# Kernel tuning notes

Hardware: AMD Instinct MI355X
Metric: run time of the kernel (lower is better)

The kernel has to match this reference:

```python
import jax, jax.numpy as jnp
import numpy as np

N_RAYS, N_SAMPLES, N_VERTS = 2048, 32, 6890

def setup_inputs() -> dict:
    key = jax.random.key(0)
    k1, k2, k3, k4 = jax.random.split(key, 4)
    rays_points_world = jax.random.normal(k1, (1, N_RAYS, 1, N_SAMPLES, 3), jnp.float32)
    rays_directions_world = jax.random.normal(k2, (1, N_RAYS, 1, N_SAMPLES, 3), jnp.float32)
    vertices_posed = jax.random.normal(k3, (1, N_VERTS, 3), jnp.float32)
    # Ts must be invertible: small perturbation of identity (like rigid bone transforms)
    Ts = jax.random.normal(k4, (1, N_VERTS, 4, 4), jnp.float32) * 0.1 + jnp.eye(4, dtype=jnp.float32)
    return {
        'rays_points_world': rays_points_world,
        'rays_directions_world': rays_directions_world,
        'vertices_posed': vertices_posed,
        'Ts': Ts,
    }

def reference(rays_points_world, rays_directions_world, vertices_posed, Ts):
    orig_shape = rays_points_world.shape  # [1, R, 1, S, 3]
    pts = rays_points_world.reshape(-1, 3)          # (N, 3), N = R*S
    verts = vertices_posed[0]                       # (V, 3)
    # squared Euclidean distances via expansion (avoids N x V x 3 intermediate)
    d2 = ((pts * pts).sum(-1, keepdims=True)
          - 2.0 * (pts @ verts.T)
          + (verts * verts).sum(-1)[None, :])       # (N, V)
    idx = jnp.argmin(d2, axis=-1)                   # (N,) nearest vertex per point
    T_inv = jnp.linalg.inv(Ts)[0]                   # (V, 4, 4)
    T_sel = T_inv[idx]                              # (N, 4, 4) gather
    # flip x,y signs, build homogeneous coords
    xyz = jnp.stack([-pts[:, 0], -pts[:, 1], pts[:, 2]], axis=-1)      # (N, 3)
    homo = jnp.concatenate([xyz, jnp.ones_like(xyz[:, :1])], axis=-1)  # (N, 4)
    can = jnp.einsum('nij,nj->ni', T_sel, homo)[:, :3]                 # (N, 3)
    can = can.reshape(orig_shape)                                      # [1, R, 1, S, 3]
    # direction = finite diff along sample axis, last repeated
    dirs = can[..., 1:, :] - can[..., :-1, :]
    dirs = jnp.concatenate([dirs, dirs[..., -1:, :]], axis=-2)
    norm = jnp.linalg.norm(dirs, axis=-1, keepdims=True)
    dirs = dirs / jnp.maximum(norm, 1e-12)  # matches torch F.normalize eps
    flip = jnp.array([-1.0, -1.0, 1.0], dtype=can.dtype)
    return can * flip, dirs * flip
```

## Files before the change

kernel.cpp:

```cpp
#include <hip/hip_runtime.h>
#include <math.h>
#include <stdint.h>

#define N_RAYS    2048
#define N_SAMPLES 32
#define NPTS      (N_RAYS * N_SAMPLES)
#define NV        6890
#define G         32
#define NCELLS    (G * G * G)
#define SPLIT     8
#define RMAX      3
#define QMASK     0xFFFFE000u
#define IMASK     0x1FFFu
#define CMASK     0x1FFFu

#define TIE_REL   3e-3f
#define TIE_ABS   2e-5f

#define WS_COUNT     0
#define WS_FBC       4
#define WS_PARAMS    16
#define WS_HIST      128
#define WS_ROWMASK   (WS_HIST + 4 * NCELLS)
#define WS_CELLINFO  (WS_ROWMASK + 4 * G * G)
#define WS_SVERTS    (WS_CELLINFO + 4 * NCELLS)
#define WS_ORIGIDX   (WS_SVERTS + 16 * NV)
#define WS_LIST      (WS_ORIGIDX + 2 * NV + 12)
#define WS_NEEDED    (WS_LIST + 2 * NPTS)
#define WS_IDX       WS_HIST
#define WS_ZERO_W    ((WS_CELLINFO) / 4)

__device__ __forceinline__ uint64_t umin64(uint64_t a, uint64_t b) { return a < b ? a : b; }
__device__ __forceinline__ uint64_t umax64(uint64_t a, uint64_t b) { return a < b ? b : a; }

__global__ __launch_bounds__(256) void init_kernel(const float* __restrict__ verts,
                                                   float* __restrict__ params,
                                                   uint32_t* __restrict__ wzero) {
    const int t = threadIdx.x;
    if (blockIdx.x != 0) {
        for (int i = (blockIdx.x - 1) * 256 + t; i < WS_ZERO_W; i += (gridDim.x - 1) * 256) {
            if (i >= 4 && i < 32) continue;
            wzero[i] = 0u;
        }
        return;
    }
    __shared__ float mn[3][256], mx[3][256];
    float lmn[3] = {1e30f, 1e30f, 1e30f}, lmx[3] = {-1e30f, -1e30f, -1e30f};
    for (int v = t; v < NV; v += 256) {
        #pragma unroll
        for (int d = 0; d < 3; ++d) {
            float x = verts[v * 3 + d];
            lmn[d] = fminf(lmn[d], x); lmx[d] = fmaxf(lmx[d], x);
        }
    }
    #pragma unroll
    for (int d = 0; d < 3; ++d) { mn[d][t] = lmn[d]; mx[d][t] = lmx[d]; }
    __syncthreads();
    for (int s = 128; s > 0; s >>= 1) {
        if (t < s) {
            #pragma unroll
            for (int d = 0; d < 3; ++d) {
                mn[d][t] = fminf(mn[d][t], mn[d][t + s]);
                mx[d][t] = fmaxf(mx[d][t], mx[d][t + s]);
            }
        }
        __syncthreads();
    }
    if (t == 0) {
        #pragma unroll
        for (int d = 0; d < 3; ++d) {
            const float lo = mn[d][0] - 1e-3f, hi = mx[d][0] + 1e-3f;
            const float span = fmaxf(hi - lo, 1e-2f);
            params[d]     = lo;
            params[3 + d] = span / (float)G;
            params[6 + d] = (float)G / span;
        }
    }
}

__device__ __forceinline__ int cell_clamp(float x, float org, float ih) {
    int c = (int)floorf((x - org) * ih);
    return min(max(c, 0), G - 1);
}

__global__ void hist_kernel(const float* __restrict__ verts, const float* __restrict__ params,
                            uint32_t* __restrict__ hist) {
    const int v = blockIdx.x * blockDim.x + threadIdx.x;
    if (v >= NV) return;
    const int cx = cell_clamp(verts[v * 3 + 0], params[0], params[6]);
    const int cy = cell_clamp(verts[v * 3 + 1], params[1], params[7]);
    const int cz = cell_clamp(verts[v * 3 + 2], params[2], params[8]);
    atomicAdd(&hist[(cz * G + cy) * G + cx], 1u);
}

__global__ __launch_bounds__(1024) void scan_cells_kernel(const uint32_t* __restrict__ hist,
                                                          uint32_t* __restrict__ cellinfo,
                                                          uint32_t* __restrict__ rowmask) {
    __shared__ uint32_t part[1024];
    const int t = threadIdx.x;
    uint32_t loc[32];
    uint32_t sum = 0, rmask = 0;
    const int base = t * 32;
    #pragma unroll
    for (int i = 0; i < 32; ++i) {
        const uint32_t h = hist[base + i];
        loc[i] = sum; sum += h;
        if (h) rmask |= (1u << i);
    }
    part[t] = sum;
    rowmask[t] = rmask;
    __syncthreads();
    for (int off = 1; off < 1024; off <<= 1) {
        const uint32_t v = (t >= off) ? part[t - off] : 0u;
        __syncthreads();
        part[t] += v;
        __syncthreads();
    }
    const uint32_t pre = (t == 0) ? 0u : part[t - 1];
    #pragma unroll
    for (int i = 0; i < 32; ++i) {
        const uint32_t nxt = (i == 31) ? sum : loc[i + 1];
        const uint32_t cnt = nxt - loc[i];
        cellinfo[base + i] = ((pre + loc[i]) << 13) | cnt;
    }
}

__global__ void scatter_kernel(const float* __restrict__ verts, const float* __restrict__ params,
                               uint32_t* __restrict__ hist, const uint32_t* __restrict__ cellinfo,
                               float4* __restrict__ sverts, uint16_t* __restrict__ origidx) {
    const int v = blockIdx.x * blockDim.x + threadIdx.x;
    if (v >= NV) return;
    const float x = verts[v * 3 + 0], y = verts[v * 3 + 1], z = verts[v * 3 + 2];
    const int cx = cell_clamp(x, params[0], params[6]);
    const int cy = cell_clamp(y, params[1], params[7]);
    const int cz = cell_clamp(z, params[2], params[8]);
    const int c = (cz * G + cy) * G + cx;
    const uint32_t old = atomicSub(&hist[c], 1u);
    const uint32_t pos = (cellinfo[c] >> 13) + old - 1u;
    sverts[pos] = make_float4(x, y, z, fmaf(x, x, fmaf(y, y, z * z)));
    origidx[pos] = (uint16_t)v;
}

__global__ __launch_bounds__(256) void search_kernel(
    const float* __restrict__ pts, const float* __restrict__ params,
    const uint32_t* __restrict__ rowmask, const uint32_t* __restrict__ cellinfo,
    const float4* __restrict__ sverts, const uint16_t* __restrict__ origidx,
    uint16_t* __restrict__ idx16, uint16_t* __restrict__ list16,
    uint32_t* __restrict__ count, uint32_t* __restrict__ fbcount)
{
    __shared__ uint32_t srow[G * G];
    const int tid = threadIdx.x;
    for (int i = tid; i < G * G; i += 256) srow[i] = rowmask[i];
    __syncthreads();

    const int gtid = blockIdx.x * 256 + tid;
    const int sub  = gtid & (SPLIT - 1);
    const int n    = gtid / SPLIT;
    const float px = pts[n * 3 + 0], py = pts[n * 3 + 1], pz = pts[n * 3 + 2];
    const float acc = -0.5f * fmaf(px, px, fmaf(py, py, pz * pz));
    const float org0 = params[0], org1 = params[1], org2 = params[2];
    const float h0 = params[3], h1 = params[4], h2 = params[5];
    const int cx = cell_clamp(px, org0, params[6]);
    const int cy = cell_clamp(py, org1, params[7]);
    const int cz = cell_clamp(pz, org2, params[8]);

    uint32_t k1 = ~0u, k2 = ~0u;
    bool unproven = true;

    for (int r = 0; r <= RMAX; ++r) {
        const int xlo = max(cx - r, 0), xhi = min(cx + r, G - 1);
        const int ylo = max(cy - r, 0), yhi = min(cy + r, G - 1);
        const int zlo = max(cz - r, 0), zhi = min(cz + r, G - 1);
        const uint32_t wm = (uint32_t)((((uint64_t)1 << (xhi - xlo + 1)) - 1) << xlo);
        for (int z = zlo; z <= zhi; ++z) {
            const int az = abs(z - cz);
            for (int y = ylo; y <= yhi; ++y) {
                const int row = z * G + y;
                const int ayz = max(abs(y - cy), az);
                if (ayz == r) {
                    if (!(srow[row] & wm)) continue;
                    const uint32_t i0 = cellinfo[row * G + xlo];
                    const uint32_t i1 = cellinfo[row * G + xhi];
                    const uint32_t s = i0 >> 13;
                    const uint32_t e = (i1 >> 13) + (i1 & CMASK);
                    for (uint32_t j = s + sub; j < e; j += SPLIT) {
                        const float4 q = sverts[j];
                        const float dot = fmaf(px, q.x, fmaf(py, q.y, fmaf(pz, q.z, acc)));
                        const float d = fmaxf(fmaf(-2.f, dot, q.w), 0.f);
                        const uint32_t k = (__float_as_uint(d) & QMASK) | j;
                        k2 = min(k2, max(k1, k)); k1 = min(k1, k);
                    }
                } else {
                    #pragma unroll
                    for (int side = 0; side < 2; ++side) {
                        const int x = side ? cx + r : cx - r;
                        if (x < 0 || x > G - 1) continue;
                        if (!((srow[row] >> x) & 1u)) continue;
                        const uint32_t info = cellinfo[row * G + x];
                        const uint32_t s = info >> 13;
                        const uint32_t e = s + (info & CMASK);
                        for (uint32_t j = s + sub; j < e; j += SPLIT) {
                            const float4 q = sverts[j];
                            const float dot = fmaf(px, q.x, fmaf(py, q.y, fmaf(pz, q.z, acc)));
                            const float d = fmaxf(fmaf(-2.f, dot, q.w), 0.f);
                            const uint32_t k = (__float_as_uint(d) & QMASK) | j;
                            k2 = min(k2, max(k1, k)); k1 = min(k1, k);
                        }
                    }
                }
            }
        }
        uint32_t m1 = k1;
        #pragma unroll
        for (int off = 1; off < SPLIT; off <<= 1)
            m1 = min(m1, (uint32_t)__shfl_xor((int)m1, off));
        if (m1 != ~0u) {
            float dmin = 1e30f;
            bool any = false;
            if (xlo > 0)     { dmin = fminf(dmin, px - fmaf((float)xlo,     h0, org0)); any = true; }
            if (xhi < G - 1) { dmin = fminf(dmin, fmaf((float)(xhi + 1), h0, org0) - px); any = true; }
            if (ylo > 0)     { dmin = fminf(dmin, py - fmaf((float)ylo,     h1, org1)); any = true; }
            if (yhi < G - 1) { dmin = fminf(dmin, fmaf((float)(yhi + 1), h1, org1) - py); any = true; }
            if (zlo > 0)     { dmin = fminf(dmin, pz - fmaf((float)zlo,     h2, org2)); any = true; }
            if (zhi < G - 1) { dmin = fminf(dmin, fmaf((float)(zhi + 1), h2, org2) - pz); any = true; }
            if (!any) { unproven = false; break; }
            const float dout = fmaxf(dmin, 0.f);
            const float d1f = __uint_as_float(m1 & QMASK);
            if (dout * dout > fmaf(d1f, 1.05f, 1e-3f)) { unproven = false; break; }
        }
    }

    #pragma unroll
    for (int off = 1; off < SPLIT; off <<= 1) {
        const uint32_t o1 = (uint32_t)__shfl_xor((int)k1, off);
        const uint32_t o2 = (uint32_t)__shfl_xor((int)k2, off);
        k2 = min(min(k2, o2), max(k1, o1)); k1 = min(k1, o1);
    }

    if (sub == 0) {
        if (unproven) {
            const uint32_t p = atomicAdd(fbcount, 1u);
            list16[NPTS - 1 - p] = (uint16_t)n;
        } else {
            const float d1 = __uint_as_float(k1 & QMASK);
            const float d2 = __uint_as_float(k2 & QMASK);
            idx16[n] = origidx[k1 & IMASK];
            if (d2 - d1 < fmaf(TIE_REL, d1, TIE_ABS)) {
                const uint32_t p = atomicAdd(count, 1u);
                list16[p] = (uint16_t)n;
            }
        }
    }
}

__global__ __launch_bounds__(256) void fixup_kernel(
    const float* __restrict__ pts,
    const float4* __restrict__ sverts, const uint16_t* __restrict__ origidx,
    uint16_t* __restrict__ list16,
    const uint32_t* __restrict__ count, const uint32_t* __restrict__ fbcount,
    uint16_t* __restrict__ idx16)
{
    const uint32_t fcnt = *fbcount;
    const uint32_t tcnt = *count;
    const uint32_t total = fcnt + tcnt;
    const int wv = threadIdx.x >> 6, lane = threadIdx.x & 63;
    for (uint32_t jj = blockIdx.x * 4 + wv; jj < total; jj += gridDim.x * 4) {
        const bool isFb = jj < fcnt;
        const int n = isFb ? (int)list16[NPTS - 1 - jj] : (int)list16[jj - fcnt];
        const float px = pts[n * 3 + 0], py = pts[n * 3 + 1], pz = pts[n * 3 + 2];
        bool needF64 = true;
        if (isFb) {
            const float acc = -0.5f * fmaf(px, px, fmaf(py, py, pz * pz));
            uint32_t k1 = ~0u, k2 = ~0u;
            int v = lane;
            for (; v + 192 < NV; v += 256) {
                const float4 q0 = sverts[v];
                const float4 q1 = sverts[v + 64];
                const float4 q2 = sverts[v + 128];
                const float4 q3 = sverts[v + 192];
                float dot, d; uint32_t k;
                dot = fmaf(px, q0.x, fmaf(py, q0.y, fmaf(pz, q0.z, acc)));
                d = fmaxf(fmaf(-2.f, dot, q0.w), 0.f);
                k = (__float_as_uint(d) & QMASK) | (uint32_t)v;
                k2 = min(k2, max(k1, k)); k1 = min(k1, k);
                dot = fmaf(px, q1.x, fmaf(py, q1.y, fmaf(pz, q1.z, acc)));
                d = fmaxf(fmaf(-2.f, dot, q1.w), 0.f);
                k = (__float_as_uint(d) & QMASK) | (uint32_t)(v + 64);
                k2 = min(k2, max(k1, k)); k1 = min(k1, k);
                dot = fmaf(px, q2.x, fmaf(py, q2.y, fmaf(pz, q2.z, acc)));
                d = fmaxf(fmaf(-2.f, dot, q2.w), 0.f);
                k = (__float_as_uint(d) & QMASK) | (uint32_t)(v + 128);
                k2 = min(k2, max(k1, k)); k1 = min(k1, k);
                dot = fmaf(px, q3.x, fmaf(py, q3.y, fmaf(pz, q3.z, acc)));
                d = fmaxf(fmaf(-2.f, dot, q3.w), 0.f);
                k = (__float_as_uint(d) & QMASK) | (uint32_t)(v + 192);
                k2 = min(k2, max(k1, k)); k1 = min(k1, k);
            }
            for (; v < NV; v += 64) {
                const float4 q = sverts[v];
                const float dot = fmaf(px, q.x, fmaf(py, q.y, fmaf(pz, q.z, acc)));
                const float d = fmaxf(fmaf(-2.f, dot, q.w), 0.f);
                const uint32_t k = (__float_as_uint(d) & QMASK) | (uint32_t)v;
                k2 = min(k2, max(k1, k)); k1 = min(k1, k);
            }
            #pragma unroll
            for (int off = 1; off < 64; off <<= 1) {
                const uint32_t o1 = (uint32_t)__shfl_xor((int)k1, off);
                const uint32_t o2 = (uint32_t)__shfl_xor((int)k2, off);
                k2 = min(min(k2, o2), max(k1, o1)); k1 = min(k1, o1);
            }
            const float d1 = __uint_as_float(k1 & QMASK);
            const float d2 = __uint_as_float(k2 & QMASK);
            needF64 = (d2 - d1 < fmaf(TIE_REL, d1, TIE_ABS));
            if (!needF64 && lane == 0) idx16[n] = origidx[k1 & IMASK];
        }
        if (needF64) {
            const double pxd = (double)px, pyd = (double)py, pzd = (double)pz;
            double best = 1e300; uint32_t bi = 0xFFFFFFFFu;
            int v = lane;
            for (; v + 192 < NV; v += 256) {
                const float4 q0 = sverts[v];
                const float4 q1 = sverts[v + 64];
                const float4 q2 = sverts[v + 128];
                const float4 q3 = sverts[v + 192];
                const uint32_t o0 = origidx[v];
                const uint32_t o1 = origidx[v + 64];
                const uint32_t o2 = origidx[v + 128];
                const uint32_t o3 = origidx[v + 192];
                double dx, dy, dz, d;
                dx = pxd - (double)q0.x; dy = pyd - (double)q0.y; dz = pzd - (double)q0.z;
                d = dx*dx + dy*dy + dz*dz;
                if (d < best || (d == best && o0 < bi)) { best = d; bi = o0; }
                dx = pxd - (double)q1.x; dy = pyd - (double)q1.y; dz = pzd - (double)q1.z;
                d = dx*dx + dy*dy + dz*dz;
                if (d < best || (d == best && o1 < bi)) { best = d; bi = o1; }
                dx = pxd - (double)q2.x; dy = pyd - (double)q2.y; dz = pzd - (double)q2.z;
                d = dx*dx + dy*dy + dz*dz;
                if (d < best || (d == best && o2 < bi)) { best = d; bi = o2; }
                dx = pxd - (double)q3.x; dy = pyd - (double)q3.y; dz = pzd - (double)q3.z;
                d = dx*dx + dy*dy + dz*dz;
                if (d < best || (d == best && o3 < bi)) { best = d; bi = o3; }
            }
            for (; v < NV; v += 64) {
                const float4 q = sverts[v];
                const uint32_t oi = origidx[v];
                const double dx = pxd - (double)q.x;
                const double dy = pyd - (double)q.y;
                const double dz = pzd - (double)q.z;
                const double d = dx*dx + dy*dy + dz*dz;
                if (d < best || (d == best && oi < bi)) { best = d; bi = oi; }
            }
            #pragma unroll
            for (int off = 1; off < 64; off <<= 1) {
                const double od = __shfl_xor(best, off);
                const uint32_t oi = (uint32_t)__shfl_xor((int)bi, off);
                if (od < best || (od == best && oi < bi)) { best = od; bi = oi; }
            }
            if (lane == 0) idx16[n] = (uint16_t)bi;
        }
    }
}

__global__ __launch_bounds__(256) void output_kernel(
    const float* __restrict__ pts, const float* __restrict__ Ts,
    const uint16_t* __restrict__ idx16, float* __restrict__ out)
{
    __shared__ double sc[256][3];
    const int tid = threadIdx.x;
    const int n = blockIdx.x * 256 + tid;
    const float px = pts[n*3+0], py = pts[n*3+1], pz = pts[n*3+2];
    const int v = (int)idx16[n];

    const float4* T4 = reinterpret_cast<const float4*>(Ts + (size_t)v * 16);
    const float4 r0 = T4[0], r1 = T4[1], r2 = T4[2], r3 = T4[3];
    const double m[16] = { r0.x, r0.y, r0.z, r0.w,  r1.x, r1.y, r1.z, r1.w,
                           r2.x, r2.y, r2.z, r2.w,  r3.x, r3.y, r3.z, r3.w };
    double inv[16];
    inv[0]  =  m[5]*m[10]*m[15] - m[5]*m[11]*m[14] - m[9]*m[6]*m[15] + m[9]*m[7]*m[14] + m[13]*m[6]*m[11] - m[13]*m[7]*m[10];
    inv[4]  = -m[4]*m[10]*m[15] + m[4]*m[11]*m[14] + m[8]*m[6]*m[15] - m[8]*m[7]*m[14] - m[12]*m[6]*m[11] + m[12]*m[7]*m[10];
    inv[8]  =  m[4]*m[9]*m[15] - m[4]*m[11]*m[13] - m[8]*m[5]*m[15] + m[8]*m[7]*m[13] + m[12]*m[5]*m[11] - m[12]*m[7]*m[9];
    inv[12] = -m[4]*m[9]*m[14] + m[4]*m[10]*m[13] + m[8]*m[5]*m[14] - m[8]*m[6]*m[13] - m[12]*m[5]*m[10] + m[12]*m[6]*m[9];
    inv[1]  = -m[1]*m[10]*m[15] + m[1]*m[11]*m[14] + m[9]*m[2]*m[15] - m[9]*m[3]*m[14] - m[13]*m[2]*m[11] + m[13]*m[3]*m[10];
    inv[5]  =  m[0]*m[10]*m[15] - m[0]*m[11]*m[14] - m[8]*m[2]*m[15] + m[8]*m[3]*m[14] + m[12]*m[2]*m[11] - m[12]*m[3]*m[10];
    inv[9]  = -m[0]*m[9]*m[15] + m[0]*m[11]*m[13] + m[8]*m[1]*m[15] - m[8]*m[3]*m[13] - m[12]*m[1]*m[11] + m[12]*m[3]*m[9];
    inv[13] =  m[0]*m[9]*m[14] - m[0]*m[10]*m[13] - m[8]*m[1]*m[14] + m[8]*m[2]*m[13] + m[12]*m[1]*m[10] - m[12]*m[2]*m[9];
    inv[2]  =  m[1]*m[6]*m[15] - m[1]*m[7]*m[14] - m[5]*m[2]*m[15] + m[5]*m[3]*m[14] + m[13]*m[2]*m[7] - m[13]*m[3]*m[6];
    inv[6]  = -m[0]*m[6]*m[15] + m[0]*m[7]*m[14] + m[4]*m[2]*m[15] - m[4]*m[3]*m[14] - m[12]*m[2]*m[7] + m[12]*m[3]*m[6];
    inv[10] =  m[0]*m[5]*m[15] - m[0]*m[7]*m[13] - m[4]*m[1]*m[15] + m[4]*m[3]*m[13] + m[12]*m[1]*m[7] - m[12]*m[3]*m[5];
    inv[14] = -m[0]*m[5]*m[14] + m[0]*m[6]*m[13] + m[4]*m[1]*m[14] - m[4]*m[2]*m[13] - m[12]*m[1]*m[6] + m[12]*m[2]*m[5];
    inv[3]  = -m[1]*m[6]*m[11] + m[1]*m[7]*m[10] + m[5]*m[2]*m[11] - m[5]*m[3]*m[10] - m[9]*m[2]*m[7] + m[9]*m[3]*m[6];
    inv[7]  =  m[0]*m[6]*m[11] - m[0]*m[7]*m[10] - m[4]*m[2]*m[11] + m[4]*m[3]*m[10] + m[8]*m[2]*m[7] - m[8]*m[3]*m[6];
    inv[11] = -m[0]*m[5]*m[11] + m[0]*m[7]*m[9] + m[4]*m[1]*m[11] - m[4]*m[3]*m[9] - m[8]*m[1]*m[7] + m[8]*m[3]*m[5];
    inv[15] =  m[0]*m[5]*m[10] - m[0]*m[6]*m[9] - m[4]*m[1]*m[10] + m[4]*m[2]*m[9] + m[8]*m[1]*m[6] - m[8]*m[2]*m[5];
    const double det = m[0]*inv[0] + m[1]*inv[4] + m[2]*inv[8] + m[3]*inv[12];
    const double rd = 1.0 / det;

    const double hx = -(double)px, hy = -(double)py, hz = (double)pz;
    const double c0 = (inv[0]*hx + inv[1]*hy + inv[2]*hz  + inv[3])  * rd;
    const double c1 = (inv[4]*hx + inv[5]*hy + inv[6]*hz  + inv[7])  * rd;
    const double c2 = (inv[8]*hx + inv[9]*hy + inv[10]*hz + inv[11]) * rd;
    const double f0 = -c0, f1 = -c1, f2 = c2;

    out[n*3+0] = (float)f0; out[n*3+1] = (float)f1; out[n*3+2] = (float)f2;
    sc[tid][0] = f0; sc[tid][1] = f1; sc[tid][2] = f2;
    __syncthreads();

    int l0 = tid, l1 = tid + 1;
    if ((tid & (N_SAMPLES - 1)) == N_SAMPLES - 1) { l0 = tid - 1; l1 = tid; }
    const double dx = sc[l1][0] - sc[l0][0];
    const double dy = sc[l1][1] - sc[l0][1];
    const double dz = sc[l1][2] - sc[l0][2];
    const double nr = fmax(sqrt(dx*dx + dy*dy + dz*dz), 1e-12);
    float* o = out + (size_t)NPTS * 3 + (size_t)n * 3;
    o[0] = (float)(dx / nr); o[1] = (float)(dy / nr); o[2] = (float)(dz / nr);
}

__global__ void zero_kernel(uint32_t* __restrict__ w, int nwords) {
    for (int i = blockIdx.x * blockDim.x + threadIdx.x; i < nwords; i += gridDim.x * blockDim.x)
        w[i] = 0u;
}

__global__ __launch_bounds__(256) void scan_kernel(
    const float* __restrict__ pts, const float* __restrict__ verts,
    uint16_t* __restrict__ idx16, uint16_t* __restrict__ list16,
    uint32_t* __restrict__ count)
{
    __shared__ float4 sv[2048];
    const int tid  = threadIdx.x;
    const int part = tid & 7;
    const int grp  = tid >> 3;
    const int n0   = blockIdx.x * 64 + grp * 2;
    const float ax = pts[n0*3+0], ay = pts[n0*3+1], az = pts[n0*3+2];
    const float bx = pts[n0*3+3], by = pts[n0*3+4], bz = pts[n0*3+5];
    const float acc = -0.5f * fmaf(ax, ax, fmaf(ay, ay, az*az));
    const float bcc = -0.5f * fmaf(bx, bx, fmaf(by, by, bz*bz));
    uint64_t ak1 = ~0ull, ak2 = ~0ull, bk1 = ~0ull, bk2 = ~0ull;
    for (int base = 0; base < NV; base += 2048) {
        const int cnt = min(NV - base, 2048);
        __syncthreads();
        for (int v = tid; v < cnt; v += 256) {
            const float x = verts[(base+v)*3+0], y = verts[(base+v)*3+1], z = verts[(base+v)*3+2];
            sv[v] = make_float4(x, y, z, fmaf(x, x, fmaf(y, y, z*z)));
        }
        __syncthreads();
        #pragma unroll 4
        for (int v = part; v < cnt; v += 8) {
            const float4 q = sv[v];
            const uint64_t vi = (uint64_t)(base + v);
            float s, d; uint64_t k;
            s = fmaf(ax, q.x, fmaf(ay, q.y, fmaf(az, q.z, acc)));
            d = fmaxf(fmaf(-2.f, s, q.w), 0.f);
            k = ((uint64_t)__float_as_uint(d) << 32) | vi;
            ak2 = umin64(ak2, umax64(ak1, k)); ak1 = umin64(ak1, k);
            s = fmaf(bx, q.x, fmaf(by, q.y, fmaf(bz, q.z, bcc)));
            d = fmaxf(fmaf(-2.f, s, q.w), 0.f);
            k = ((uint64_t)__float_as_uint(d) << 32) | vi;
            bk2 = umin64(bk2, umax64(bk1, k)); bk1 = umin64(bk1, k);
        }
    }
    #pragma unroll
    for (int off = 1; off < 8; off <<= 1) {
        uint64_t o1, o2;
        o1 = __shfl_xor((unsigned long long)ak1, off); o2 = __shfl_xor((unsigned long long)ak2, off);
        ak2 = umin64(umin64(ak2, o2), umax64(ak1, o1)); ak1 = umin64(ak1, o1);
        o1 = __shfl_xor((unsigned long long)bk1, off); o2 = __shfl_xor((unsigned long long)bk2, off);
        bk2 = umin64(umin64(bk2, o2), umax64(bk1, o1)); bk1 = umin64(bk1, o1);
    }
    if (part == 0) {
        const float ad1 = __uint_as_float((uint32_t)(ak1 >> 32));
        const float ad2 = __uint_as_float((uint32_t)(ak2 >> 32));
        idx16[n0] = (uint16_t)(ak1 & 0xFFFFu);
        if (ad2 - ad1 < fmaf(1e-4f, ad1, TIE_ABS)) { uint32_t p = atomicAdd(count, 1u); list16[p] = (uint16_t)n0; }
        const float bd1 = __uint_as_float((uint32_t)(bk1 >> 32));
        const float bd2 = __uint_as_float((uint32_t)(bk2 >> 32));
        idx16[n0+1] = (uint16_t)(bk1 & 0xFFFFu);
        if (bd2 - bd1 < fmaf(1e-4f, bd1, TIE_ABS)) { uint32_t p = atomicAdd(count, 1u); list16[p] = (uint16_t)(n0+1); }
    }
}

__global__ __launch_bounds__(256) void refine_kernel(
    const float* __restrict__ pts, const float* __restrict__ verts,
    const uint16_t* __restrict__ list16, const uint32_t* __restrict__ count,
    uint16_t* __restrict__ idx16)
{
    const uint32_t cnt = *count;
    const int wv = threadIdx.x >> 6, lane = threadIdx.x & 63;
    for (uint32_t j = blockIdx.x * 4 + wv; j < cnt; j += gridDim.x * 4) {
        const int n = (int)list16[j];
        const double px = (double)pts[n*3+0];
        const double py = (double)pts[n*3+1];
        const double pz = (double)pts[n*3+2];
        double best = 1e300; uint32_t bi = 0xFFFFFFFFu;
        for (int v = lane; v < NV; v += 64) {
            const double dx = px - (double)verts[v*3+0];
            const double dy = py - (double)verts[v*3+1];
            const double dz = pz - (double)verts[v*3+2];
            const double d = dx*dx + dy*dy + dz*dz;
            if (d < best || (d == best && (uint32_t)v < bi)) { best = d; bi = (uint32_t)v; }
        }
        #pragma unroll
        for (int off = 1; off < 64; off <<= 1) {
            const double od = __shfl_xor(best, off);
            const uint32_t oi = (uint32_t)__shfl_xor((int)bi, off);
            if (od < best || (od == best && oi < bi)) { best = od; bi = oi; }
        }
        if (lane == 0) idx16[n] = (uint16_t)bi;
    }
}

extern "C" void kernel_launch(void* const* d_in, const int* in_sizes, int n_in,
                              void* d_out, int out_size, void* d_ws, size_t ws_size,
                              hipStream_t stream) {
    const float* pts   = (const float*)d_in[0];
    const float* verts = (const float*)d_in[2];
    const float* Ts    = (const float*)d_in[3];
    float* out = (float*)d_out;

    uint8_t* ws = (uint8_t*)d_ws;
    uint32_t* count   = (uint32_t*)(ws + WS_COUNT);
    uint32_t* fbcount = (uint32_t*)(ws + WS_FBC);

    if (ws_size >= (size_t)WS_NEEDED) {
        float*    params   = (float*)(ws + WS_PARAMS);
        uint32_t* hist     = (uint32_t*)(ws + WS_HIST);
        uint32_t* rowmask  = (uint32_t*)(ws + WS_ROWMASK);
        uint32_t* cellinfo = (uint32_t*)(ws + WS_CELLINFO);
        float4*   sverts   = (float4*)(ws + WS_SVERTS);
        uint16_t* origidx  = (uint16_t*)(ws + WS_ORIGIDX);
        uint16_t* idx16    = (uint16_t*)(ws + WS_IDX);
        uint16_t* list16   = (uint16_t*)(ws + WS_LIST);
        const int vblocks = (NV + 255) / 256;

        hipLaunchKernelGGL(init_kernel, dim3(65), dim3(256), 0, stream,
                           verts, params, (uint32_t*)ws);
        hipLaunchKernelGGL(hist_kernel, dim3(vblocks), dim3(256), 0, stream,
                           verts, params, hist);
        hipLaunchKernelGGL(scan_cells_kernel, dim3(1), dim3(1024), 0, stream,
                           hist, cellinfo, rowmask);
        hipLaunchKernelGGL(scatter_kernel, dim3(vblocks), dim3(256), 0, stream,
                           verts, params, hist, cellinfo, sverts, origidx);
        hipLaunchKernelGGL(search_kernel, dim3(NPTS * SPLIT / 256), dim3(256), 0, stream,
                           pts, params, rowmask, cellinfo, sverts, origidx,
                           idx16, list16, count, fbcount);
        hipLaunchKernelGGL(fixup_kernel, dim3(1024), dim3(256), 0, stream,
                           pts, sverts, origidx, list16, count, fbcount, idx16);
        hipLaunchKernelGGL(output_kernel, dim3(NPTS / 256), dim3(256), 0, stream,
                           pts, Ts, idx16, out);
    } else {
        uint16_t* idx16  = (uint16_t*)(ws + 64);
        uint16_t* list16 = (uint16_t*)(ws + 64 + 2 * NPTS);
        hipLaunchKernelGGL(zero_kernel, dim3(1), dim3(64), 0, stream, (uint32_t*)ws, 1);
        hipLaunchKernelGGL(scan_kernel, dim3(NPTS / 64), dim3(256), 0, stream,
                           pts, verts, idx16, list16, count);
        hipLaunchKernelGGL(refine_kernel, dim3(512), dim3(256), 0, stream,
                           pts, verts, list16, count, idx16);
        hipLaunchKernelGGL(output_kernel, dim3(NPTS / 256), dim3(256), 0, stream,
                           pts, Ts, idx16, out);
    }
}
```

Before: 85.74 us.

## Widen per-point split to 16 lanes and search grid in two shell stages

Each query point is now scanned by 16 lanes instead of 8, and the radius-by-radius shell search (r=0..3) becomes two stages. The first stage scans the 3x3x3 neighbourhood and checks whether the nearest vertex is proven. Only if not does a second stage scan the 7x7x7 box, skipping the already-scanned core. This cuts per-radius shuffle reductions and the loop overhead from the finer shells, and gives each lane fewer candidates. In exchange, unproven points scan the whole r=3 box at once, and the wider split doubles the thread count and adds a shuffle step to each reduction.

New measurement: 95.18 us. +11.0%, slower.

```diff
diff --git a/kernel.cpp b/kernel.cpp
--- a/kernel.cpp
+++ b/kernel.cpp
@@ -8,8 +8,7 @@
 #define NV        6890
 #define G         32
 #define NCELLS    (G * G * G)
-#define SPLIT     8
-#define RMAX      3
+#define SPLIT     16
 #define QMASK     0xFFFFE000u
 #define IMASK     0x1FFFu
 #define CMASK     0x1FFFu
@@ -32,6 +31,9 @@
 
 __device__ __forceinline__ uint64_t umin64(uint64_t a, uint64_t b) { return a < b ? a : b; }
 __device__ __forceinline__ uint64_t umax64(uint64_t a, uint64_t b) { return a < b ? b : a; }
+__device__ __forceinline__ uint32_t wmask(int a, int b) {
+    return (uint32_t)((((uint64_t)1 << (b - a + 1)) - 1) << a);
+}
 
 __global__ __launch_bounds__(256) void init_kernel(const float* __restrict__ verts,
                                                    float* __restrict__ params,
@@ -167,67 +169,72 @@
     uint32_t k1 = ~0u, k2 = ~0u;
     bool unproven = true;
 
-    for (int r = 0; r <= RMAX; ++r) {
-        const int xlo = max(cx - r, 0), xhi = min(cx + r, G - 1);
-        const int ylo = max(cy - r, 0), yhi = min(cy + r, G - 1);
-        const int zlo = max(cz - r, 0), zhi = min(cz + r, G - 1);
-        const uint32_t wm = (uint32_t)((((uint64_t)1 << (xhi - xlo + 1)) - 1) << xlo);
-        for (int z = zlo; z <= zhi; ++z) {
-            const int az = abs(z - cz);
-            for (int y = ylo; y <= yhi; ++y) {
-                const int row = z * G + y;
-                const int ayz = max(abs(y - cy), az);
-                if (ayz == r) {
-                    if (!(srow[row] & wm)) continue;
-                    const uint32_t i0 = cellinfo[row * G + xlo];
-                    const uint32_t i1 = cellinfo[row * G + xhi];
-                    const uint32_t s = i0 >> 13;
-                    const uint32_t e = (i1 >> 13) + (i1 & CMASK);
-                    for (uint32_t j = s + sub; j < e; j += SPLIT) {
-                        const float4 q = sverts[j];
-                        const float dot = fmaf(px, q.x, fmaf(py, q.y, fmaf(pz, q.z, acc)));
-                        const float d = fmaxf(fmaf(-2.f, dot, q.w), 0.f);
-                        const uint32_t k = (__float_as_uint(d) & QMASK) | j;
-                        k2 = min(k2, max(k1, k)); k1 = min(k1, k);
-                    }
-                } else {
-                    #pragma unroll
-                    for (int side = 0; side < 2; ++side) {
-                        const int x = side ? cx + r : cx - r;
-                        if (x < 0 || x > G - 1) continue;
-                        if (!((srow[row] >> x) & 1u)) continue;
-                        const uint32_t info = cellinfo[row * G + x];
-                        const uint32_t s = info >> 13;
-                        const uint32_t e = s + (info & CMASK);
-                        for (uint32_t j = s + sub; j < e; j += SPLIT) {
-                            const float4 q = sverts[j];
-                            const float dot = fmaf(px, q.x, fmaf(py, q.y, fmaf(pz, q.z, acc)));
-                            const float d = fmaxf(fmaf(-2.f, dot, q.w), 0.f);
-                            const uint32_t k = (__float_as_uint(d) & QMASK) | j;
-                            k2 = min(k2, max(k1, k)); k1 = min(k1, k);
-                        }
-                    }
-                }
-            }
-        }
+    auto scan_run = [&](int rowG, int a, int b) {
+        const uint32_t i0 = cellinfo[rowG + a];
+        const uint32_t i1 = cellinfo[rowG + b];
+        const uint32_t s = i0 >> 13;
+        const uint32_t e = (i1 >> 13) + (i1 & CMASK);
+        for (uint32_t j = s + sub; j < e; j += SPLIT) {
+            const float4 q = sverts[j];
+            const float dot = fmaf(px, q.x, fmaf(py, q.y, fmaf(pz, q.z, acc)));
+            const float d = fmaxf(fmaf(-2.f, dot, q.w), 0.f);
+            const uint32_t k = (__float_as_uint(d) & QMASK) | j;
+            k2 = min(k2, max(k1, k)); k1 = min(k1, k);
+        }
+    };
+    auto proven = [&](int xl, int xh, int yl, int yh, int zl, int zh) -> bool {
         uint32_t m1 = k1;
         #pragma unroll
         for (int off = 1; off < SPLIT; off <<= 1)
             m1 = min(m1, (uint32_t)__shfl_xor((int)m1, off));
-        if (m1 != ~0u) {
-            float dmin = 1e30f;
-            bool any = false;
-            if (xlo > 0)     { dmin = fminf(dmin, px - fmaf((float)xlo,     h0, org0)); any = true; }
-            if (xhi < G - 1) { dmin = fminf(dmin, fmaf((float)(xhi + 1), h0, org0) - px); any = true; }
-            if (ylo > 0)     { dmin = fminf(dmin, py - fmaf((float)ylo,     h1, org1)); any = true; }
-            if (yhi < G - 1) { dmin = fminf(dmin, fmaf((float)(yhi + 1), h1, org1) - py); any = true; }
-            if (zlo > 0)     { dmin = fminf(dmin, pz - fmaf((float)zlo,     h2, org2)); any = true; }
-            if (zhi < G - 1) { dmin = fminf(dmin, fmaf((float)(zhi + 1), h2, org2) - pz); any = true; }
-            if (!any) { unproven = false; break; }
-            const float dout = fmaxf(dmin, 0.f);
-            const float d1f = __uint_as_float(m1 & QMASK);
-            if (dout * dout > fmaf(d1f, 1.05f, 1e-3f)) { unproven = false; break; }
-        }
+        if (m1 == ~0u) return false;
+        float dmin = 1e30f;
+        bool any = false;
+        if (xl > 0)     { dmin = fminf(dmin, px - fmaf((float)xl,      h0, org0)); any = true; }
+        if (xh < G - 1) { dmin = fminf(dmin, fmaf((float)(xh + 1), h0, org0) - px); any = true; }
+        if (yl > 0)     { dmin = fminf(dmin, py - fmaf((float)yl,      h1, org1)); any = true; }
+        if (yh < G - 1) { dmin = fminf(dmin, fmaf((float)(yh + 1), h1, org1) - py); any = true; }
+        if (zl > 0)     { dmin = fminf(dmin, pz - fmaf((float)zl,      h2, org2)); any = true; }
+        if (zh < G - 1) { dmin = fminf(dmin, fmaf((float)(zh + 1), h2, org2) - pz); any = true; }
+        if (!any) return true;
+        const float dout = fmaxf(dmin, 0.f);
+        const float d1f = __uint_as_float(m1 & QMASK);
+        return dout * dout > fmaf(d1f, 1.05f, 1e-3f);
+    };
+
+    const int xlo1 = max(cx - 1, 0), xhi1 = min(cx + 1, G - 1);
+    const int ylo1 = max(cy - 1, 0), yhi1 = min(cy + 1, G - 1);
+    const int zlo1 = max(cz - 1, 0), zhi1 = min(cz + 1, G - 1);
+    const uint32_t wm1 = wmask(xlo1, xhi1);
+    for (int z = zlo1; z <= zhi1; ++z)
+        for (int y = ylo1; y <= yhi1; ++y) {
+            const int row = z * G + y;
+            if (srow[row] & wm1) scan_run(row * G, xlo1, xhi1);
+        }
+    if (proven(xlo1, xhi1, ylo1, yhi1, zlo1, zhi1)) {
+        unproven = false;
+    } else {
+        const int xlo3 = max(cx - 3, 0), xhi3 = min(cx + 3, G - 1);
+        const int ylo3 = max(cy - 3, 0), yhi3 = min(cy + 3, G - 1);
+        const int zlo3 = max(cz - 3, 0), zhi3 = min(cz + 3, G - 1);
+        const uint32_t wm3 = wmask(xlo3, xhi3);
+        for (int z = zlo3; z <= zhi3; ++z) {
+            const bool zin = (z >= zlo1 && z <= zhi1);
+            for (int y = ylo3; y <= yhi3; ++y) {
+                const int row = z * G + y;
+                const uint32_t rm = srow[row];
+                if (!(rm & wm3)) continue;
+                if (zin && y >= ylo1 && y <= yhi1) {
+                    if (xlo3 <= xlo1 - 1 && (rm & wmask(xlo3, xlo1 - 1)))
+                        scan_run(row * G, xlo3, xlo1 - 1);
+                    if (xhi1 + 1 <= xhi3 && (rm & wmask(xhi1 + 1, xhi3)))
+                        scan_run(row * G, xhi1 + 1, xhi3);
+                } else {
+                    scan_run(row * G, xlo3, xhi3);
+                }
+            }
+        }
+        if (proven(xlo3, xhi3, ylo3, yhi3, zlo3, zhi3)) unproven = false;
     }
 
     #pragma unroll
```

## Fuse grid build stages into a single one-block kernel

Applied to the files above, without the earlier changes.

Merges the init/bounds, histogram, cell scan and scatter kernels into one 1024-thread single-block kernel. The bounds reduction now uses wave shuffles, and the scatter uses per-cell start offsets with atomicAdd instead of atomicSub. Each vertex's cell index is cached in list16 scratch so it is computed only once. This removes three kernel launches and their inter-kernel gaps, but runs the histogram and scatter on a single workgroup, which serializes work that previously spread across many blocks.

After: 118.0 us. 1.38x slower.

```diff
diff --git a/kernel.cpp b/kernel.cpp
--- a/kernel.cpp
+++ b/kernel.cpp
@@ -13,6 +13,7 @@
 #define QMASK     0xFFFFE000u
 #define IMASK     0x1FFFu
 #define CMASK     0x1FFFu
+#define BT        1024
 
 #define TIE_REL   3e-3f
 #define TIE_ABS   2e-5f
@@ -28,76 +29,76 @@
 #define WS_LIST      (WS_ORIGIDX + 2 * NV + 12)
 #define WS_NEEDED    (WS_LIST + 2 * NPTS)
 #define WS_IDX       WS_HIST
-#define WS_ZERO_W    ((WS_CELLINFO) / 4)
 
 __device__ __forceinline__ uint64_t umin64(uint64_t a, uint64_t b) { return a < b ? a : b; }
 __device__ __forceinline__ uint64_t umax64(uint64_t a, uint64_t b) { return a < b ? b : a; }
 
-__global__ __launch_bounds__(256) void init_kernel(const float* __restrict__ verts,
-                                                   float* __restrict__ params,
-                                                   uint32_t* __restrict__ wzero) {
+__device__ __forceinline__ int cell_clamp(float x, float org, float ih) {
+    int c = (int)floorf((x - org) * ih);
+    return min(max(c, 0), G - 1);
+}
+
+__global__ __launch_bounds__(BT) void build_kernel(
+    const float* __restrict__ verts, float* __restrict__ params,
+    uint32_t* __restrict__ hist, uint32_t* __restrict__ cellinfo,
+    uint32_t* __restrict__ rowmask, float4* __restrict__ sverts,
+    uint16_t* __restrict__ origidx, uint16_t* __restrict__ cellscratch,
+    uint32_t* __restrict__ counters)
+{
+    __shared__ float spm[12];
+    __shared__ float redmn[16][3], redmx[16][3];
+    __shared__ uint32_t part[BT];
     const int t = threadIdx.x;
-    if (blockIdx.x != 0) {
-        for (int i = (blockIdx.x - 1) * 256 + t; i < WS_ZERO_W; i += (gridDim.x - 1) * 256) {
-            if (i >= 4 && i < 32) continue;
-            wzero[i] = 0u;
-        }
-        return;
-    }
-    __shared__ float mn[3][256], mx[3][256];
-    float lmn[3] = {1e30f, 1e30f, 1e30f}, lmx[3] = {-1e30f, -1e30f, -1e30f};
-    for (int v = t; v < NV; v += 256) {
+    const int lane = t & 63, wv = t >> 6;
+
+    float mnv[3] = {1e30f, 1e30f, 1e30f}, mxv[3] = {-1e30f, -1e30f, -1e30f};
+    for (int v = t; v < NV; v += BT) {
         #pragma unroll
         for (int d = 0; d < 3; ++d) {
-            float x = verts[v * 3 + d];
-            lmn[d] = fminf(lmn[d], x); lmx[d] = fmaxf(lmx[d], x);
+            const float x = verts[v * 3 + d];
+            mnv[d] = fminf(mnv[d], x); mxv[d] = fmaxf(mxv[d], x);
         }
     }
     #pragma unroll
-    for (int d = 0; d < 3; ++d) { mn[d][t] = lmn[d]; mx[d][t] = lmx[d]; }
-    __syncthreads();
-    for (int s = 128; s > 0; s >>= 1) {
-        if (t < s) {
-            #pragma unroll
-            for (int d = 0; d < 3; ++d) {
-                mn[d][t] = fminf(mn[d][t], mn[d][t + s]);
-                mx[d][t] = fmaxf(mx[d][t], mx[d][t + s]);
-            }
-        }
-        __syncthreads();
-    }
+    for (int off = 32; off > 0; off >>= 1) {
+        #pragma unroll
+        for (int d = 0; d < 3; ++d) {
+            mnv[d] = fminf(mnv[d], __shfl_xor(mnv[d], off));
+            mxv[d] = fmaxf(mxv[d], __shfl_xor(mxv[d], off));
+        }
+    }
+    if (lane == 0) {
+        #pragma unroll
+        for (int d = 0; d < 3; ++d) { redmn[wv][d] = mnv[d]; redmx[wv][d] = mxv[d]; }
+    }
+    __syncthreads();
     if (t == 0) {
         #pragma unroll
         for (int d = 0; d < 3; ++d) {
-            const float lo = mn[d][0] - 1e-3f, hi = mx[d][0] + 1e-3f;
+            float mn = redmn[0][d], mx = redmx[0][d];
+            for (int w = 1; w < 16; ++w) {
+                mn = fminf(mn, redmn[w][d]); mx = fmaxf(mx, redmx[w][d]);
+            }
+            const float lo = mn - 1e-3f, hi = mx + 1e-3f;
             const float span = fmaxf(hi - lo, 1e-2f);
-            params[d]     = lo;
-            params[3 + d] = span / (float)G;
-            params[6 + d] = (float)G / span;
-        }
-    }
-}
-
-__device__ __forceinline__ int cell_clamp(float x, float org, float ih) {
-    int c = (int)floorf((x - org) * ih);
-    return min(max(c, 0), G - 1);
-}
-
-__global__ void hist_kernel(const float* __restrict__ verts, const float* __restrict__ params,
-                            uint32_t* __restrict__ hist) {
-    const int v = blockIdx.x * blockDim.x + threadIdx.x;
-    if (v >= NV) return;
-    const int cx = cell_clamp(verts[v * 3 + 0], params[0], params[6]);
-    const int cy = cell_clamp(verts[v * 3 + 1], params[1], params[7]);
-    const int cz = cell_clamp(verts[v * 3 + 2], params[2], params[8]);
-    atomicAdd(&hist[(cz * G + cy) * G + cx], 1u);
-}
-
-__global__ __launch_bounds__(1024) void scan_cells_kernel(const uint32_t* __restrict__ hist,
-                                                          uint32_t* __restrict__ cellinfo,
-                                                          uint32_t* __restrict__ rowmask) {
-    __shared__ uint32_t part[1024];
-    const int t = threadIdx.x;
+            spm[d] = lo; spm[3 + d] = span / (float)G; spm[6 + d] = (float)G / span;
+            params[d] = spm[d]; params[3 + d] = spm[3 + d]; params[6 + d] = spm[6 + d];
+        }
+        counters[0] = 0u; counters[1] = 0u;
+    }
+    for (int i = t; i < NCELLS; i += BT) hist[i] = 0u;
+    __syncthreads();
+
+    for (int v = t; v < NV; v += BT) {
+        const int cx = cell_clamp(verts[v * 3 + 0], spm[0], spm[6]);
+        const int cy = cell_clamp(verts[v * 3 + 1], spm[1], spm[7]);
+        const int cz = cell_clamp(verts[v * 3 + 2], spm[2], spm[8]);
+        const int c = (cz * G + cy) * G + cx;
+        cellscratch[v] = (uint16_t)c;
+        atomicAdd(&hist[c], 1u);
+    }
+    __syncthreads();
+
     uint32_t loc[32];
     uint32_t sum = 0, rmask = 0;
     const int base = t * 32;
@@ -110,7 +111,7 @@
     part[t] = sum;
     rowmask[t] = rmask;
     __syncthreads();
-    for (int off = 1; off < 1024; off <<= 1) {
+    for (int off = 1; off < BT; off <<= 1) {
         const uint32_t v = (t >= off) ? part[t - off] : 0u;
         __syncthreads();
         part[t] += v;
@@ -121,24 +122,19 @@
     for (int i = 0; i < 32; ++i) {
         const uint32_t nxt = (i == 31) ? sum : loc[i + 1];
         const uint32_t cnt = nxt - loc[i];
-        cellinfo[base + i] = ((pre + loc[i]) << 13) | cnt;
-    }
-}
-
-__global__ void scatter_kernel(const float* __restrict__ verts, const float* __restrict__ params,
-                               uint32_t* __restrict__ hist, const uint32_t* __restrict__ cellinfo,
-                               float4* __restrict__ sverts, uint16_t* __restrict__ origidx) {
-    const int v = blockIdx.x * blockDim.x + threadIdx.x;
-    if (v >= NV) return;
-    const float x = verts[v * 3 + 0], y = verts[v * 3 + 1], z = verts[v * 3 + 2];
-    const int cx = cell_clamp(x, params[0], params[6]);
-    const int cy = cell_clamp(y, params[1], params[7]);
-    const int cz = cell_clamp(z, params[2], params[8]);
-    const int c = (cz * G + cy) * G + cx;
-    const uint32_t old = atomicSub(&hist[c], 1u);
-    const uint32_t pos = (cellinfo[c] >> 13) + old - 1u;
-    sverts[pos] = make_float4(x, y, z, fmaf(x, x, fmaf(y, y, z * z)));
-    origidx[pos] = (uint16_t)v;
+        const uint32_t st  = pre + loc[i];
+        cellinfo[base + i] = (st << 13) | cnt;
+        hist[base + i] = st;
+    }
+    __syncthreads();
+
+    for (int v = t; v < NV; v += BT) {
+        const int c = (int)cellscratch[v];
+        const uint32_t pos = atomicAdd(&hist[c], 1u);
+        const float x = verts[v * 3 + 0], y = verts[v * 3 + 1], z = verts[v * 3 + 2];
+        sverts[pos] = make_float4(x, y, z, fmaf(x, x, fmaf(y, y, z * z)));
+        origidx[pos] = (uint16_t)v;
+    }
 }
 
 __global__ __launch_bounds__(256) void search_kernel(
@@ -529,16 +525,10 @@
         uint16_t* origidx  = (uint16_t*)(ws + WS_ORIGIDX);
         uint16_t* idx16    = (uint16_t*)(ws + WS_IDX);
         uint16_t* list16   = (uint16_t*)(ws + WS_LIST);
-        const int vblocks = (NV + 255) / 256;
-
-        hipLaunchKernelGGL(init_kernel, dim3(65), dim3(256), 0, stream,
-                           verts, params, (uint32_t*)ws);
-        hipLaunchKernelGGL(hist_kernel, dim3(vblocks), dim3(256), 0, stream,
-                           verts, params, hist);
-        hipLaunchKernelGGL(scan_cells_kernel, dim3(1), dim3(1024), 0, stream,
-                           hist, cellinfo, rowmask);
-        hipLaunchKernelGGL(scatter_kernel, dim3(vblocks), dim3(256), 0, stream,
-                           verts, params, hist, cellinfo, sverts, origidx);
+
+        hipLaunchKernelGGL(build_kernel, dim3(1), dim3(BT), 0, stream,
+                           verts, params, hist, cellinfo, rowmask,
+                           sverts, origidx, list16, (uint32_t*)ws);
         hipLaunchKernelGGL(search_kernel, dim3(NPTS * SPLIT / 256), dim3(256), 0, stream,
                            pts, params, rowmask, cellinfo, sverts, origidx,
                            idx16, list16, count, fbcount);
```
